# Kernel tuning notes

Measured on AMD Instinct MI355X. Metric: run time of the kernel, lower is better.

The kernel has to match this reference:

```python
import jax, jax.numpy as jnp
import numpy as np

B, C, H, W = 16, 512, 64, 64


def setup_inputs() -> dict:
    key = jax.random.key(0)
    ks = jax.random.split(key, 5)
    s = 0.02  # init scale for projection weights
    return {
        "x": jax.random.normal(ks[0], (B, C, H, W), jnp.float32),
        "Wqkv": jax.random.normal(ks[1], (3 * C, C), jnp.float32) * s,
        "bqkv": jnp.zeros((3 * C,), jnp.float32),
        "Wm": jax.random.normal(ks[2], (2 * C, C), jnp.float32) * s,
        "bm": jnp.zeros((2 * C,), jnp.float32),
        "Wg": jax.random.normal(ks[3], (C, 2 * C), jnp.float32) * s,
        "bg": jnp.zeros((C,), jnp.float32),
        "Wr": jax.random.normal(ks[4], (C, C), jnp.float32) * s,
        "br": jnp.zeros((C,), jnp.float32),
    }


def reference(x, Wqkv, bqkv, Wm, bm, Wg, bg, Wr, br):
    b, c, h, w = x.shape
    n = h * w
    xf = x.reshape(b, c, n)  # [B,C,N]
    # qkv projection: [B,3C,N] -> q,k,v each [B,C,N]
    qkv = jnp.einsum('oc,bcn->bon', Wqkv, xf) + bqkv[None, :, None]
    q, k, v = qkv[:, :c], qkv[:, c:2 * c], qkv[:, 2 * c:]
    # modulation from v: mq, mk each [B,C,N]
    mqk = jnp.einsum('oc,bcn->bon', Wm, v) + bm[None, :, None]
    mq, mk = mqk[:, :c], mqk[:, c:]
    _q = jax.nn.softmax(-jax.nn.relu(q * mq), axis=-1)   # softmax over N
    _k = jax.nn.relu(k * mk)                             # [B,C,N]
    # channel attention: [B,C,N] @ [B,N,C] -> [B,C,C]
    scores = jnp.einsum('bcn,bdn->bcd', _q, _k) / jnp.sqrt(jnp.float32(c))
    attn = jax.nn.softmax(scores, axis=-1)
    y = jnp.einsum('bcd,bdn->bcn', attn, v)              # [B,C,N]
    y2d = y.reshape(b, c, h, w)
    # gated residual: g = sigmoid(W_g @ cat(y, x))
    catf = jnp.concatenate([y, xf], axis=1)              # [B,2C,N]
    g = jax.nn.sigmoid(jnp.einsum('oc,bcn->bon', Wg, catf) + bg[None, :, None]).reshape(b, c, h, w)
    r = (jnp.einsum('oc,bcn->bon', Wr, xf) + br[None, :, None]).reshape(b, c, h, w)
    out = g * r + (1.0 - g) * y2d
    return (out, attn)
```

## Files before the change

kernel.cpp:

```cpp
#include <hip/hip_runtime.h>
#include <math.h>

#define Bb 16
#define Cc 512
#define Nn 4096
#define CN (512L * 4096)

typedef __bf16 bf16x8 __attribute__((ext_vector_type(8)));
typedef float  floatx4 __attribute__((ext_vector_type(4)));

__device__ __forceinline__ unsigned short f2bf(float f) {
    unsigned int u = __float_as_uint(f);
    unsigned int r = (u + 0x7FFFu + ((u >> 16) & 1u)) >> 16;
    return (unsigned short)r;
}
__device__ __forceinline__ float bf2f(unsigned short s) {
    return __uint_as_float(((unsigned int)s) << 16);
}

__device__ __forceinline__ void gload16(const void* g, void* l) {
    __builtin_amdgcn_global_load_lds(
        (const __attribute__((address_space(1))) unsigned int*)g,
        (__attribute__((address_space(3))) unsigned int*)l,
        16, 0, 0);
}

template<int OUTF32, int SPLIT>
__global__ __launch_bounds__(256) void gemm_bt(
    const unsigned short* __restrict__ A1,
    const unsigned short* __restrict__ A2, int lda, int asplit,
    const unsigned short* __restrict__ B, int ldb,
    const float* __restrict__ bias,
    void* __restrict__ Cv, int ldc,
    int K, float scale,
    long sA, long sB, long sC)
{
    __shared__ __align__(16) unsigned short Alds[2][8 * 512];
    __shared__ __align__(16) unsigned short Blds[2][8 * 512];

    const int t    = threadIdx.x;
    const int lane = t & 63;
    const int wave = t >> 6;
    const int m0 = blockIdx.y * 128;
    const int n0 = blockIdx.x * 128;
    const int wm = (wave >> 1) * 64;
    const int wn = (wave & 1) * 64;

    const unsigned short* Ab1 = A1 + (size_t)blockIdx.z * sA;
    const unsigned short* Ab2 = SPLIT ? (A2 + (size_t)blockIdx.z * sA) : nullptr;
    const unsigned short* Bb_ = B + (size_t)blockIdx.z * sB;

    const int srow = lane & 15;
    const int sk   = (lane >> 4) * 8;
    const int sub0 = wave * 2;

    const unsigned short* gA0 = Ab1 + (size_t)(m0 + (sub0    ) * 16 + srow) * lda + sk;
    const unsigned short* gA1 = Ab1 + (size_t)(m0 + (sub0 + 1) * 16 + srow) * lda + sk;
    const unsigned short* gB0 = Bb_ + (size_t)(n0 + (sub0    ) * 16 + srow) * ldb + sk;
    const unsigned short* gB1 = Bb_ + (size_t)(n0 + (sub0 + 1) * 16 + srow) * ldb + sk;
    const ptrdiff_t sjump = SPLIT ? (Ab2 - Ab1) - (ptrdiff_t)asplit : 0;

    auto stage = [&](int buf, int k0) {
        const unsigned short* a0 = gA0 + k0;
        const unsigned short* a1 = gA1 + k0;
        if (SPLIT && k0 >= asplit) { a0 += sjump; a1 += sjump; }
        gload16(a0,       &Alds[buf][(sub0    ) * 512]);
        gload16(gB0 + k0, &Blds[buf][(sub0    ) * 512]);
        gload16(a1,       &Alds[buf][(sub0 + 1) * 512]);
        gload16(gB1 + k0, &Blds[buf][(sub0 + 1) * 512]);
    };

    floatx4 acc[4][4] = {};

    const int nt = K >> 5;
    int cur = 0;
    stage(0, 0);

    for (int ti = 0; ti < nt; ++ti) {
        if (ti + 1 < nt) {
            stage(cur ^ 1, (ti + 1) << 5);
            asm volatile("s_waitcnt vmcnt(4)" ::: "memory");
        } else {
            asm volatile("s_waitcnt vmcnt(0)" ::: "memory");
        }
        __builtin_amdgcn_s_barrier();
        __builtin_amdgcn_sched_barrier(0);

        bf16x8 af[4], bfr[4];
#pragma unroll
        for (int i = 0; i < 4; ++i) {
            af[i]  = *(const bf16x8*)&Alds[cur][((wm >> 4) + i) * 512 + lane * 8];
            bfr[i] = *(const bf16x8*)&Blds[cur][((wn >> 4) + i) * 512 + lane * 8];
        }
        __builtin_amdgcn_s_setprio(1);
#pragma unroll
        for (int i = 0; i < 4; ++i)
#pragma unroll
            for (int j = 0; j < 4; ++j)
                acc[i][j] = __builtin_amdgcn_mfma_f32_16x16x32_bf16(af[i], bfr[j], acc[i][j], 0, 0, 0);
        __builtin_amdgcn_s_setprio(0);

        asm volatile("s_waitcnt lgkmcnt(0)" ::: "memory");
        __builtin_amdgcn_s_barrier();
        __builtin_amdgcn_sched_barrier(0);
        cur ^= 1;
    }

    const int rbase = (lane >> 4) * 4;
    const int cofs  = lane & 15;
#pragma unroll
    for (int j = 0; j < 4; ++j) {
        int col = n0 + wn + j * 16 + cofs;
        float bv = bias ? bias[col] : 0.0f;
#pragma unroll
        for (int i = 0; i < 4; ++i) {
#pragma unroll
            for (int r = 0; r < 4; ++r) {
                int row = m0 + wm + i * 16 + rbase + r;
                float v = acc[i][j][r] * scale + bv;
                if (OUTF32) {
                    float* C = (float*)Cv + (size_t)blockIdx.z * sC;
                    C[(size_t)row * ldc + col] = v;
                } else {
                    unsigned short* C = (unsigned short*)Cv + (size_t)blockIdx.z * sC;
                    C[(size_t)row * ldc + col] = f2bf(v);
                }
            }
        }
    }
}

__global__ __launch_bounds__(256) void wcast(const float* __restrict__ w,
                                             unsigned short* __restrict__ o, int n)
{
    int i = (blockIdx.x * 256 + threadIdx.x) * 4;
    float4 v = *(const float4*)&w[i];
    ushort4 u;
    u.x = f2bf(v.x); u.y = f2bf(v.y); u.z = f2bf(v.z); u.w = f2bf(v.w);
    *(ushort4*)&o[i] = u;
}

__global__ __launch_bounds__(256) void transpose_x(const float* __restrict__ x,
                                                   unsigned short* __restrict__ xp)
{
    __shared__ unsigned short tile[64][65];
    const float* X = x + (size_t)blockIdx.z * CN;
    unsigned short* O = xp + (size_t)blockIdx.z * CN;
    int n0 = blockIdx.x * 64, c0 = blockIdx.y * 64;
    int tq = (threadIdx.x & 15) * 4, tr = threadIdx.x >> 4;
#pragma unroll
    for (int r = 0; r < 4; ++r) {
        int cl = tr + r * 16;
        float4 v = *(const float4*)&X[(size_t)(c0 + cl) * 4096 + n0 + tq];
        tile[tq + 0][cl] = f2bf(v.x);
        tile[tq + 1][cl] = f2bf(v.y);
        tile[tq + 2][cl] = f2bf(v.z);
        tile[tq + 3][cl] = f2bf(v.w);
    }
    __syncthreads();
#pragma unroll
    for (int r = 0; r < 4; ++r) {
        int nl = tr + r * 16;
        ushort4 o;
        o.x = tile[nl][tq + 0]; o.y = tile[nl][tq + 1];
        o.z = tile[nl][tq + 2]; o.w = tile[nl][tq + 3];
        *(ushort4*)&O[(size_t)(n0 + nl) * 512 + c0 + tq] = o;
    }
}

__global__ __launch_bounds__(256) void qk_transform(
    const unsigned short* __restrict__ qkv, const unsigned short* __restrict__ mqk,
    unsigned short* __restrict__ T, int coff, int neg)
{
    __shared__ __align__(8) unsigned short tile[64][68];
    const unsigned short* S1 = qkv + (size_t)blockIdx.z * (4096L * 1536) + coff;
    const unsigned short* S2 = mqk + (size_t)blockIdx.z * (4096L * 1024) + coff;
    unsigned short* O = T + (size_t)blockIdx.z * CN;
    int n0 = blockIdx.x * 64, c0 = blockIdx.y * 64;
    int tq = (threadIdx.x & 15) * 4, tr = threadIdx.x >> 4;
#pragma unroll
    for (int r = 0; r < 4; ++r) {
        int nl = tr + r * 16;
        ushort4 a = *(const ushort4*)&S1[(size_t)(n0 + nl) * 1536 + c0 + tq];
        ushort4 m = *(const ushort4*)&S2[(size_t)(n0 + nl) * 1024 + c0 + tq];
        float f0 = fmaxf(bf2f(a.x) * bf2f(m.x), 0.0f);
        float f1 = fmaxf(bf2f(a.y) * bf2f(m.y), 0.0f);
        float f2 = fmaxf(bf2f(a.z) * bf2f(m.z), 0.0f);
        float f3 = fmaxf(bf2f(a.w) * bf2f(m.w), 0.0f);
        if (neg) { f0 = -f0; f1 = -f1; f2 = -f2; f3 = -f3; }
        ushort4 p;
        p.x = f2bf(f0); p.y = f2bf(f1); p.z = f2bf(f2); p.w = f2bf(f3);
        *(ushort4*)&tile[nl][tq] = p;
    }
    __syncthreads();
#pragma unroll
    for (int r = 0; r < 4; ++r) {
        int cl = tr + r * 16;
        ushort4 o;
        o.x = tile[tq + 0][cl]; o.y = tile[tq + 1][cl];
        o.z = tile[tq + 2][cl]; o.w = tile[tq + 3][cl];
        *(ushort4*)&O[(size_t)(c0 + cl) * 4096 + n0 + tq] = o;
    }
}

__global__ __launch_bounds__(256) void qsoftmax_bf(unsigned short* __restrict__ Q)
{
    unsigned short* p = Q + (size_t)blockIdx.x * 4096;
    const int t = threadIdx.x;
    const int lane = t & 63;
    const int wv = t >> 6;
    __shared__ float red[8];

    float vals[16];
    float mx = -1e30f;
#pragma unroll
    for (int i = 0; i < 16; ++i) {
        float v = bf2f(p[t + i * 256]);
        vals[i] = v;
        mx = fmaxf(mx, v);
    }
#pragma unroll
    for (int off = 32; off > 0; off >>= 1) mx = fmaxf(mx, __shfl_xor(mx, off));
    if (lane == 0) red[wv] = mx;
    __syncthreads();
    mx = fmaxf(fmaxf(red[0], red[1]), fmaxf(red[2], red[3]));

    float sum = 0.0f;
#pragma unroll
    for (int i = 0; i < 16; ++i) {
        vals[i] = __expf(vals[i] - mx);
        sum += vals[i];
    }
#pragma unroll
    for (int off = 32; off > 0; off >>= 1) sum += __shfl_xor(sum, off);
    if (lane == 0) red[4 + wv] = sum;
    __syncthreads();
    sum = red[4] + red[5] + red[6] + red[7];
    float inv = 1.0f / sum;
#pragma unroll
    for (int i = 0; i < 16; ++i) p[t + i * 256] = f2bf(vals[i] * inv);
}

__global__ __launch_bounds__(256) void attn_softmax_dual(
    float* __restrict__ attnf, unsigned short* __restrict__ attnb)
{
    float* p = attnf + (size_t)blockIdx.x * 512;
    unsigned short* pb = attnb + (size_t)blockIdx.x * 512;
    const int t = threadIdx.x;
    const int lane = t & 63;
    const int wv = t >> 6;
    __shared__ float red[8];

    float v0 = p[t], v1 = p[t + 256];
    float mx = fmaxf(v0, v1);
#pragma unroll
    for (int off = 32; off > 0; off >>= 1) mx = fmaxf(mx, __shfl_xor(mx, off));
    if (lane == 0) red[wv] = mx;
    __syncthreads();
    mx = fmaxf(fmaxf(red[0], red[1]), fmaxf(red[2], red[3]));

    float e0 = __expf(v0 - mx);
    float e1 = __expf(v1 - mx);
    float sum = e0 + e1;
#pragma unroll
    for (int off = 32; off > 0; off >>= 1) sum += __shfl_xor(sum, off);
    if (lane == 0) red[4 + wv] = sum;
    __syncthreads();
    sum = red[4] + red[5] + red[6] + red[7];
    float inv = 1.0f / sum;
    float a0 = e0 * inv, a1 = e1 * inv;
    p[t] = a0;        p[t + 256] = a1;
    pb[t] = f2bf(a0); pb[t + 256] = f2bf(a1);
}

__global__ __launch_bounds__(256) void final_fuse(
    const unsigned short* __restrict__ gl, const unsigned short* __restrict__ rr,
    const unsigned short* __restrict__ yy, float* __restrict__ out)
{
    __shared__ __align__(16) float tile[64][68];
    size_t bo = (size_t)blockIdx.z * CN;
    const unsigned short* G_ = gl + bo;
    const unsigned short* R_ = rr + bo;
    const unsigned short* Y_ = yy + bo;
    float* O = out + bo;
    int n0 = blockIdx.x * 64, c0 = blockIdx.y * 64;
    int tq = (threadIdx.x & 15) * 4, tr = threadIdx.x >> 4;
#pragma unroll
    for (int r = 0; r < 4; ++r) {
        int nl = tr + r * 16;
        size_t base = (size_t)(n0 + nl) * 512 + c0 + tq;
        ushort4 g4 = *(const ushort4*)&G_[base];
        ushort4 r4 = *(const ushort4*)&R_[base];
        ushort4 y4 = *(const ushort4*)&Y_[base];
        float4 o;
        float g;
        g = 1.0f / (1.0f + __expf(-bf2f(g4.x))); o.x = g * bf2f(r4.x) + (1.0f - g) * bf2f(y4.x);
        g = 1.0f / (1.0f + __expf(-bf2f(g4.y))); o.y = g * bf2f(r4.y) + (1.0f - g) * bf2f(y4.y);
        g = 1.0f / (1.0f + __expf(-bf2f(g4.z))); o.z = g * bf2f(r4.z) + (1.0f - g) * bf2f(y4.z);
        g = 1.0f / (1.0f + __expf(-bf2f(g4.w))); o.w = g * bf2f(r4.w) + (1.0f - g) * bf2f(y4.w);
        *(float4*)&tile[nl][tq] = o;
    }
    __syncthreads();
#pragma unroll
    for (int r = 0; r < 4; ++r) {
        int cl = tr + r * 16;
        float4 o;
        o.x = tile[tq + 0][cl]; o.y = tile[tq + 1][cl];
        o.z = tile[tq + 2][cl]; o.w = tile[tq + 3][cl];
        *(float4*)&O[(size_t)(c0 + cl) * 4096 + n0 + tq] = o;
    }
}

extern "C" void kernel_launch(void* const* d_in, const int* in_sizes, int n_in,
                              void* d_out, int out_size, void* d_ws, size_t ws_size,
                              hipStream_t stream)
{
    const float* x    = (const float*)d_in[0];
    const float* Wqkv = (const float*)d_in[1];
    const float* bqkv = (const float*)d_in[2];
    const float* Wm   = (const float*)d_in[3];
    const float* bm   = (const float*)d_in[4];
    const float* Wg   = (const float*)d_in[5];
    const float* bg   = (const float*)d_in[6];
    const float* Wr   = (const float*)d_in[7];
    const float* br   = (const float*)d_in[8];

    float* out      = (float*)d_out;
    float* attn_all = out + (size_t)Bb * CN;

    unsigned short* wq_bf = (unsigned short*)d_ws;
    unsigned short* wm_bf = wq_bf + 1536 * 512;
    unsigned short* wg_bf = wm_bf + 1024 * 512;
    unsigned short* wr_bf = wg_bf + 512 * 1024;
    unsigned short* dyn   = wr_bf + 512 * 512;
    const size_t fixed_bytes = (size_t)(1536 * 512 + 1024 * 512 + 512 * 1024 + 512 * 512) * 2;
    const size_t per_batch_bytes = (size_t)4096 * 4096 * 2;

    int G = 16;
    while (G > 1 && fixed_bytes + (size_t)G * per_batch_bytes > ws_size) G >>= 1;

    dim3 blk(256);
    const float inv_sqrt_c = 0.044194173824159216f;

    wcast<<<1536 * 512 / 1024, blk, 0, stream>>>(Wqkv, wq_bf, 1536 * 512);
    wcast<<<1024 * 512 / 1024, blk, 0, stream>>>(Wm,   wm_bf, 1024 * 512);
    wcast<<<512 * 1024 / 1024, blk, 0, stream>>>(Wg,   wg_bf, 512 * 1024);
    wcast<<<512 * 512  / 1024, blk, 0, stream>>>(Wr,   wr_bf, 512 * 512);

    for (int b0 = 0; b0 < Bb; b0 += G) {
        unsigned short* xp   = dyn;
        unsigned short* qkvp = xp   + (size_t)G * 4096 * 512;
        unsigned short* mqkp = qkvp + (size_t)G * 4096 * 1536;
        unsigned short* qp   = mqkp + (size_t)G * 4096 * 1024;
        unsigned short* kp   = qp   + (size_t)G * CN;
        unsigned short* yp   = mqkp;
        unsigned short* glp  = mqkp + (size_t)G * CN;
        unsigned short* rp   = qp;
        unsigned short* abf  = kp;

        const float* xg   = x + (size_t)b0 * CN;
        float* outg       = out + (size_t)b0 * CN;
        float* attng      = attn_all + (size_t)b0 * 512 * 512;

        transpose_x<<<dim3(64, 8, G), blk, 0, stream>>>(xg, xp);

        gemm_bt<0, 0><<<dim3(12, 32, G), blk, 0, stream>>>(
            xp, nullptr, 512, 0, wq_bf, 512, bqkv, qkvp, 1536,
            512, 1.0f, 4096L * 512, 0L, 4096L * 1536);

        gemm_bt<0, 0><<<dim3(8, 32, G), blk, 0, stream>>>(
            qkvp + 1024, nullptr, 1536, 0, wm_bf, 512, bm, mqkp, 1024,
            512, 1.0f, 4096L * 1536, 0L, 4096L * 1024);

        qk_transform<<<dim3(64, 8, G), blk, 0, stream>>>(qkvp, mqkp, qp, 0, 1);
        qk_transform<<<dim3(64, 8, G), blk, 0, stream>>>(qkvp, mqkp, kp, 512, 0);

        qsoftmax_bf<<<G * 512, blk, 0, stream>>>(qp);

        gemm_bt<1, 0><<<dim3(4, 4, G), blk, 0, stream>>>(
            qp, nullptr, 4096, 0, kp, 4096, nullptr, attng, 512,
            4096, inv_sqrt_c, CN, CN, 512L * 512);

        attn_softmax_dual<<<G * 512, blk, 0, stream>>>(attng, abf);

        gemm_bt<0, 0><<<dim3(4, 32, G), blk, 0, stream>>>(
            qkvp + 1024, nullptr, 1536, 0, abf, 512, nullptr, yp, 512,
            512, 1.0f, 4096L * 1536, 512L * 512, 4096L * 512);

        gemm_bt<0, 1><<<dim3(4, 32, G), blk, 0, stream>>>(
            yp, xp, 512, 512, wg_bf, 1024, bg, glp, 512,
            1024, 1.0f, 4096L * 512, 0L, 4096L * 512);

        gemm_bt<0, 0><<<dim3(4, 32, G), blk, 0, stream>>>(
            xp, nullptr, 512, 0, wr_bf, 512, br, rp, 512,
            512, 1.0f, 4096L * 512, 0L, 4096L * 512);

        final_fuse<<<dim3(64, 8, G), blk, 0, stream>>>(glp, rp, yp, outg);
    }
}
```

Measured before the change: 1.246 ms.

## Triple-buffer GEMM LDS staging and remap workgroups across XCDs

The GEMM kernel moves from double to triple buffering of its A/B LDS tiles. It now prefetches two K-tiles ahead and waits with vmcnt(8) so more global loads are in flight while MFMAs run. It also remaps the linear block index so that consecutive logical tiles land on the same XCD, which is meant to improve L2 reuse of shared A/B panels. The cost is 50% more LDS per block, which may reduce occupancy.

```diff
diff --git a/kernel.cpp b/kernel.cpp
--- a/kernel.cpp
+++ b/kernel.cpp
@@ -35,20 +35,30 @@
     int K, float scale,
     long sA, long sB, long sC)
 {
-    __shared__ __align__(16) unsigned short Alds[2][8 * 512];
-    __shared__ __align__(16) unsigned short Blds[2][8 * 512];
+    __shared__ __align__(16) unsigned short Alds[3][8 * 512];
+    __shared__ __align__(16) unsigned short Blds[3][8 * 512];
+
+    const int nwg  = gridDim.x * gridDim.y * gridDim.z;
+    const int orig = blockIdx.x + gridDim.x * (blockIdx.y + gridDim.y * blockIdx.z);
+    const int q8   = nwg >> 3, r8 = nwg & 7;
+    const int xcd  = orig & 7, sub_i = orig >> 3;
+    const int logical = (xcd < r8 ? xcd * (q8 + 1) : r8 * (q8 + 1) + (xcd - r8) * q8) + sub_i;
+    const int bx = logical % gridDim.x;
+    const int btmp = logical / gridDim.x;
+    const int by = btmp % gridDim.y;
+    const int bz = btmp / gridDim.y;
 
     const int t    = threadIdx.x;
     const int lane = t & 63;
     const int wave = t >> 6;
-    const int m0 = blockIdx.y * 128;
-    const int n0 = blockIdx.x * 128;
+    const int m0 = by * 128;
+    const int n0 = bx * 128;
     const int wm = (wave >> 1) * 64;
     const int wn = (wave & 1) * 64;
 
-    const unsigned short* Ab1 = A1 + (size_t)blockIdx.z * sA;
-    const unsigned short* Ab2 = SPLIT ? (A2 + (size_t)blockIdx.z * sA) : nullptr;
-    const unsigned short* Bb_ = B + (size_t)blockIdx.z * sB;
+    const unsigned short* Ab1 = A1 + (size_t)bz * sA;
+    const unsigned short* Ab2 = SPLIT ? (A2 + (size_t)bz * sA) : nullptr;
+    const unsigned short* Bb_ = B + (size_t)bz * sB;
 
     const int srow = lane & 15;
     const int sk   = (lane >> 4) * 8;
@@ -73,12 +83,16 @@
     floatx4 acc[4][4] = {};
 
     const int nt = K >> 5;
+    stage(0, 0);
+    if (nt > 1) stage(1, 32);
     int cur = 0;
-    stage(0, 0);
 
     for (int ti = 0; ti < nt; ++ti) {
-        if (ti + 1 < nt) {
-            stage(cur ^ 1, (ti + 1) << 5);
+        if (ti + 2 < nt) {
+            int bufn = cur + 2; if (bufn >= 3) bufn -= 3;
+            stage(bufn, (ti + 2) << 5);
+            asm volatile("s_waitcnt vmcnt(8)" ::: "memory");
+        } else if (ti + 1 < nt) {
             asm volatile("s_waitcnt vmcnt(4)" ::: "memory");
         } else {
             asm volatile("s_waitcnt vmcnt(0)" ::: "memory");
@@ -103,7 +117,7 @@
         asm volatile("s_waitcnt lgkmcnt(0)" ::: "memory");
         __builtin_amdgcn_s_barrier();
         __builtin_amdgcn_sched_barrier(0);
-        cur ^= 1;
+        cur = (cur == 2) ? 0 : cur + 1;
     }
 
     const int rbase = (lane >> 4) * 4;
@@ -119,10 +133,10 @@
                 int row = m0 + wm + i * 16 + rbase + r;
                 float v = acc[i][j][r] * scale + bv;
                 if (OUTF32) {
-                    float* C = (float*)Cv + (size_t)blockIdx.z * sC;
+                    float* C = (float*)Cv + (size_t)bz * sC;
                     C[(size_t)row * ldc + col] = v;
                 } else {
-                    unsigned short* C = (unsigned short*)Cv + (size_t)blockIdx.z * sC;
+                    unsigned short* C = (unsigned short*)Cv + (size_t)bz * sC;
                     C[(size_t)row * ldc + col] = f2bf(v);
                 }
             }
```

Result: no change. 1.230 ms (-1.3%).
